# Optimization experiments

Measured on AMD Instinct MI355X. Metric: run time of the kernel, lower is better.

## Reference

```python
import jax, jax.numpy as jnp
import numpy as np

N = 50000        # nodes
E = 800000       # edges
FEAT = 64        # cfg.feature_dim
HID = 128        # cfg.hidden_dim
G = 8            # num graphs
EPS = 1e-5       # LayerNorm eps
MIN_DEPTH, MAX_DEPTH = 0.1, 3.0


def _ln(x, g, b):
    m = jnp.mean(x, axis=-1, keepdims=True)
    v = jnp.mean((x - m) ** 2, axis=-1, keepdims=True)
    return (x - m) * jax.lax.rsqrt(v + EPS) * g + b


def setup_inputs() -> dict:
    key = jax.random.key(0)
    ks = jax.random.split(key, 32)
    f32 = jnp.float32
    inp = {}
    inp['x'] = jax.random.normal(ks[0], (N, FEAT), dtype=f32)
    inp['edge_index'] = jax.random.randint(ks[1], (2, E), 0, N)
    inp['batch'] = jnp.sort(jax.random.randint(ks[2], (N,), 0, G))
    # input_projection: Linear(FEAT,HID) + LayerNorm
    inp['in_w'] = jax.random.normal(ks[3], (FEAT, HID), dtype=f32) * (1.0 / np.sqrt(FEAT))
    inp['in_b'] = jnp.zeros((HID,), f32)
    inp['in_ln_g'] = jnp.ones((HID,), f32)
    inp['in_ln_b'] = jnp.zeros((HID,), f32)
    # epigenetics
    inp['methylation'] = jnp.zeros((HID,), f32)
    inp['histones'] = jnp.zeros((4,), f32)
    inp['log_depth'] = jnp.zeros((), f32)
    # NeuralODEFunc: 3 stacked GCNConv(HID,HID) + LayerNorms, gate MLP, residual scalar
    inp['gcn_w'] = jax.random.normal(ks[4], (3, HID, HID), dtype=f32) * (1.0 / np.sqrt(HID))
    inp['gcn_b'] = jnp.zeros((3, HID), f32)
    inp['ln_g'] = jnp.ones((3, HID), f32)
    inp['ln_b'] = jnp.zeros((3, HID), f32)
    inp['gate_w'] = jax.random.normal(ks[5], (2 * HID, HID), dtype=f32) * (1.0 / np.sqrt(2 * HID))
    inp['gate_b'] = jnp.zeros((HID,), f32)
    inp['residual_weight'] = jnp.asarray(0.1, f32)
    # output_projection: Linear(HID,HID) + LayerNorm
    inp['out_w'] = jax.random.normal(ks[6], (HID, HID), dtype=f32) * (1.0 / np.sqrt(HID))
    inp['out_b'] = jnp.zeros((HID,), f32)
    inp['out_ln_g'] = jnp.ones((HID,), f32)
    inp['out_ln_b'] = jnp.zeros((HID,), f32)
    return inp


def reference(x, edge_index, batch, in_w, in_b, in_ln_g, in_ln_b, methylation,
              histones, log_depth, gcn_w, gcn_b, ln_g, ln_b, gate_w, gate_b,
              residual_weight, out_w, out_b, out_ln_g, out_ln_b):
    n = x.shape[0]
    src, dst = edge_index[0], edge_index[1]

    # input_projection (Dropout is identity in eval)
    h = jax.nn.relu(_ln(x @ in_w + in_b, in_ln_g, in_ln_b))

    # epigenetic regulation (chromatin_accessibility goes through .item() -> constant)
    meth_sil = jnp.mean(jax.nn.sigmoid(methylation))
    hm = jax.nn.sigmoid(histones)
    act = (hm[0] + hm[2]) * 0.5
    rep = (hm[1] + hm[3]) * 0.5
    chrom = jax.lax.stop_gradient(jnp.clip(act - rep + 0.5, 0.0, 1.0))
    h = h * (chrom * (1.0 - meth_sil))

    # symmetric GCN normalization, no self loops (computed once, no grad path)
    deg = jax.ops.segment_sum(jnp.ones((E,), h.dtype), dst, num_segments=n)
    dinv = jnp.where(deg > 0, jax.lax.rsqrt(jnp.maximum(deg, 1.0)), 0.0)
    enorm = (dinv[src] * dinv[dst])[:, None]  # [E,1]

    def gcn(hh, i):
        xw = hh @ gcn_w[i]                                   # [N,H]
        agg = jax.ops.segment_sum(xw[src] * enorm, dst, num_segments=n)
        return agg + gcn_b[i]

    def ode_f(hh):
        h_orig = hh
        cur = hh
        for i in range(3):  # fixed layer count
            h_new = _ln(gcn(cur, i), ln_g[i], ln_b[i])
            if i > 0:
                gate = jax.nn.sigmoid(
                    jnp.concatenate([cur, h_new], axis=-1) @ gate_w + gate_b)
                cur = gate * h_new + (1.0 - gate) * cur
            else:
                cur = h_new
        cur = jnp.tanh(cur)
        return cur + residual_weight * h_orig

    # depth via .item() in torch -> non-differentiable constant
    depth = jax.lax.stop_gradient(
        jnp.clip(jnp.exp(log_depth), MIN_DEPTH, MAX_DEPTH))
    # single fixed RK4 step over t = linspace(0, depth, 2)
    dt = depth
    k1 = ode_f(h)
    k2 = ode_f(h + 0.5 * dt * k1)
    k3 = ode_f(h + 0.5 * dt * k2)
    k4 = ode_f(h + dt * k3)
    h_final = h + (dt / 6.0) * (k1 + 2.0 * k2 + 2.0 * k3 + k4)

    # output_projection + global_mean_pool over batch
    h_out = _ln(h_final @ out_w + out_b, out_ln_g, out_ln_b)
    cnt = jax.ops.segment_sum(jnp.ones((n,), h.dtype), batch, num_segments=G)
    pooled = jax.ops.segment_sum(h_out, batch, num_segments=G)
    return pooled / jnp.maximum(cnt, 1.0)[:, None]
```

## Files before the change

### kernel.cpp

```cpp
#include <hip/hip_runtime.h>
#include <math.h>

#define NN 50000
#define EE 800000
#define HH 128
#define FF 64
#define GG 8
#define PB 500

using short8 = __attribute__((ext_vector_type(8))) short;
using f32x4  = __attribute__((ext_vector_type(4))) float;
using f32x2  = __attribute__((ext_vector_type(2))) float;

__device__ __forceinline__ float sigm(float x){ return 1.0f/(1.0f+expf(-x)); }
__device__ __forceinline__ unsigned short f2bf(float f){
    union { float f; unsigned u; } v; v.f = f;
    unsigned r = v.u + 0x7fff + ((v.u >> 16) & 1);
    return (unsigned short)(r >> 16);
}
__device__ __forceinline__ float bf2f(unsigned short h){
    union { unsigned u; float f; } v; v.u = ((unsigned)h) << 16;
    return v.f;
}

#if __has_builtin(__builtin_amdgcn_cvt_pk_fp8_f32) && __has_builtin(__builtin_amdgcn_cvt_pk_f32_fp8)
#define FP8_HW 1
#else
#define FP8_HW 0
#endif

__device__ __forceinline__ unsigned fp8enc1_sw(float f){
    union { float fl; unsigned u; } x; x.fl = f;
    unsigned s = (x.u >> 31) << 7;
    float a = fabsf(f);
    if (!(a > 0.f)) return s;
    if (a >= 448.f) return s | 0x7E;
    if (a < 0.015625f) {
        int q = (int)(a * 512.f + 0.5f);
        if (q > 7) return s | (1u << 3);
        return s | (unsigned)q;
    }
    unsigned u = x.u + (1u << 19);
    int e32 = (int)((u >> 23) & 255) - 127;
    if (e32 < -6) { int q=(int)(a*512.f+0.5f); if(q>7)q=7; return s|(unsigned)q; }
    if (e32 > 8) return s | 0x7E;
    unsigned m = (u >> 20) & 7;
    return s | ((unsigned)(e32 + 7) << 3) | m;
}
__device__ __forceinline__ float fp8dec1_sw(unsigned v){
    unsigned s = v >> 7, e = (v >> 3) & 15, m = v & 7;
    float f;
    if (e == 0) f = (float)m * 0.001953125f;
    else { union { unsigned u; float fl; } x; x.u = ((e + 120u) << 23) | (m << 20); f = x.fl; }
    return s ? -f : f;
}
__device__ __forceinline__ unsigned char e2fp8(float a){
#if FP8_HW
    return (unsigned char)(__builtin_amdgcn_cvt_pk_fp8_f32(a, a, 0, false) & 0xFF);
#else
    return (unsigned char)fp8enc1_sw(a);
#endif
}
__device__ __forceinline__ unsigned pk4fp8(float a, float b, float c, float d){
#if FP8_HW
    unsigned p0 = (unsigned)__builtin_amdgcn_cvt_pk_fp8_f32(a, b, 0, false);
    unsigned p1 = (unsigned)__builtin_amdgcn_cvt_pk_fp8_f32(c, d, 0, false);
    return (p0 & 0xFFFFu) | ((p1 & 0xFFFFu) << 16);
#else
    return fp8enc1_sw(a) | (fp8enc1_sw(b) << 8) | (fp8enc1_sw(c) << 16) | (fp8enc1_sw(d) << 24);
#endif
}
__device__ __forceinline__ float2 d2fp8(unsigned short u){
#if FP8_HW
    f32x2 r = __builtin_amdgcn_cvt_pk_f32_fp8((int)(unsigned)u, false);
    return make_float2(r[0], r[1]);
#else
    return make_float2(fp8dec1_sw(u & 0xFF), fp8dec1_sw((u >> 8) & 0xFF));
#endif
}

__global__ void k_setup(const float* __restrict__ meth,
                        const float* __restrict__ histones,
                        const float* __restrict__ logd,
                        float* __restrict__ scal)
{
    int l = threadIdx.x;
    float s = sigm(meth[l]) + sigm(meth[l + 64]);
#pragma unroll
    for (int o = 32; o >= 1; o >>= 1) s += __shfl_xor(s, o, 64);
    if (l == 0) {
        float msil = s * (1.0f / 128.0f);
        float h0 = sigm(histones[0]), h1 = sigm(histones[1]);
        float h2 = sigm(histones[2]), h3 = sigm(histones[3]);
        float act = (h0 + h2) * 0.5f, rep = (h1 + h3) * 0.5f;
        float chrom = fminf(fmaxf(act - rep + 0.5f, 0.0f), 1.0f);
        scal[0] = chrom * (1.0f - msil);
        float d = expf(logd[0]);
        scal[1] = fminf(fmaxf(d, 0.1f), 3.0f);
    }
}

__global__ void k_pack(const float* __restrict__ W, unsigned short* __restrict__ out, int K)
{
    int i = blockIdx.x * 256 + threadIdx.x;
    if (i >= K * 128) return;
    int k = i >> 7, n = i & 127;
    int c = k >> 5, kl = k & 31, q = kl >> 3, j = kl & 7;
    int b = n >> 4, ln = n & 15;
    int lane = q * 16 + ln;
    out[((c * 8 + b) * 64 + lane) * 8 + j] = f2bf(W[i]);
}

__global__ void k_cvtx(const float* __restrict__ x, unsigned short* __restrict__ xb)
{
    size_t i = (size_t)blockIdx.x * 256 + threadIdx.x;
    if (i >= (size_t)NN * 16) return;
    float4 v = ((const float4*)x)[i];
    ushort4 o;
    o.x = f2bf(v.x); o.y = f2bf(v.y); o.z = f2bf(v.z); o.w = f2bf(v.w);
    ((ushort4*)xb)[i] = o;
}

__global__ void k_hist(const int* __restrict__ ei, int* __restrict__ hist)
{
    int e = blockIdx.x * 256 + threadIdx.x;
    if (e < EE) atomicAdd(&hist[ei[EE + e]], 1);
}

__global__ void k_dinv(const int* __restrict__ hist, float* __restrict__ dinv)
{
    int n = blockIdx.x * 256 + threadIdx.x;
    if (n < NN) {
        int d = hist[n];
        dinv[n] = d > 0 ? rsqrtf((float)d) : 0.0f;
    }
}

__global__ void k_scan_a(const int* __restrict__ hist, int* __restrict__ aux)
{
    __shared__ int sh[256];
    int b = blockIdx.x, t = threadIdx.x;
    int base = b * 1024 + t * 4;
    int s = 0;
#pragma unroll
    for (int j = 0; j < 4; ++j) { int i = base + j; if (i < NN) s += hist[i]; }
    sh[t] = s; __syncthreads();
    for (int o = 128; o >= 1; o >>= 1) { if (t < o) sh[t] += sh[t + o]; __syncthreads(); }
    if (t == 0) aux[b] = sh[0];
}

__global__ void k_scan_b(int* __restrict__ aux, int nb)
{
    if (blockIdx.x == 0 && threadIdx.x == 0) {
        int run = 0;
        for (int i = 0; i < nb; ++i) { int v = aux[i]; aux[i] = run; run += v; }
    }
}

__global__ void k_scan_c(const int* __restrict__ hist, const int* __restrict__ aux,
                         int* __restrict__ row_ptr)
{
    __shared__ int sh[256];
    int b = blockIdx.x, t = threadIdx.x;
    int base = b * 1024 + t * 4;
    int v[4]; int s = 0;
#pragma unroll
    for (int j = 0; j < 4; ++j) { int i = base + j; v[j] = (i < NN) ? hist[i] : 0; s += v[j]; }
    sh[t] = s; __syncthreads();
    for (int o = 1; o < 256; o <<= 1) {
        int x = 0; if (t >= o) x = sh[t - o];
        __syncthreads(); sh[t] += x; __syncthreads();
    }
    int run = aux[b] + sh[t] - s;
#pragma unroll
    for (int j = 0; j < 4; ++j) { int i = base + j; if (i < NN) row_ptr[i] = run; run += v[j]; }
    if (b == 0 && t == 0) row_ptr[NN] = EE;
}

__global__ void k_scatter(const int* __restrict__ ei, const float* __restrict__ dinv,
                          int* __restrict__ cursor, uint2* __restrict__ ew)
{
    int e = blockIdx.x * 256 + threadIdx.x;
    if (e >= EE) return;
    int s = ei[e], d = ei[EE + e];
    int p = atomicAdd(&cursor[d], 1);
    ew[p] = make_uint2((unsigned)(s & 0xFFFF) | ((unsigned)(d & 15) << 16),
                       __float_as_uint(dinv[s] * dinv[d]));
}

__global__ void k_bounds(const int* __restrict__ batch, int* __restrict__ st)
{
    int g = threadIdx.x;
    if (g > GG) return;
    int lo = 0, hi = NN;
    while (lo < hi) { int mid = (lo + hi) >> 1; if (batch[mid] < g) lo = mid + 1; else hi = mid; }
    st[g] = lo;
}

template<int KC, int MODE>
__global__ __launch_bounds__(256) void k_dense_mfma(
    const unsigned short* __restrict__ A, const unsigned short* __restrict__ Wp,
    const float* __restrict__ bias, const float* __restrict__ lng,
    const float* __restrict__ lnb, const float* __restrict__ scal,
    unsigned short* __restrict__ out, unsigned char* __restrict__ out8)
{
    __shared__ unsigned short Ws[KC * 4096];
    const int t = threadIdx.x;
    {
        const float4* src = (const float4*)Wp;
        float4* dst = (float4*)Ws;
#pragma unroll
        for (int i = 0; i < KC * 2; ++i) dst[t + i * 256] = src[t + i * 256];
    }
    __syncthreads();
    const int wave = t >> 6, lane = t & 63;
    const int quad = lane >> 4, ln = lane & 15;
    const int r0 = blockIdx.x * 64 + wave * 16;
    const int K = KC * 32;
    const int arow = r0 + ln;
    const bool av = arow < NN;

    f32x4 acc[8] = {};
#pragma unroll
    for (int c = 0; c < KC; ++c) {
        short8 a = {};
        if (av) a = *(const short8*)(A + (size_t)arow * K + c * 32 + quad * 8);
#pragma unroll
        for (int b = 0; b < 8; ++b) {
            short8 bb = *(const short8*)&Ws[((c * 8 + b) * 64 + lane) * 8];
            acc[b] = __builtin_amdgcn_mfma_f32_16x16x32_bf16(a, bb, acc[b], 0, 0, 0);
        }
    }

    float b_s[8], g_s[8], e_s[8];
#pragma unroll
    for (int b = 0; b < 8; ++b) {
        int col = b * 16 + ln;
        b_s[b] = bias[col]; g_s[b] = lng[col]; e_s[b] = lnb[col];
    }
    float sc = (MODE == 1) ? scal[0] : 0.0f;
#pragma unroll
    for (int i = 0; i < 4; ++i) {
        int row = r0 + quad * 4 + i;
        float v[8]; float s = 0.f, q = 0.f;
#pragma unroll
        for (int b = 0; b < 8; ++b) { float x = acc[b][i] + b_s[b]; v[b] = x; s += x; q += x * x; }
#pragma unroll
        for (int o = 1; o < 16; o <<= 1) { s += __shfl_xor(s, o, 64); q += __shfl_xor(q, o, 64); }
        float m  = s * (1.0f / 128.0f);
        float vr = q * (1.0f / 128.0f) - m * m;
        float rs = rsqrtf(vr + 1e-5f);
        if (row < NN) {
#pragma unroll
            for (int b = 0; b < 8; ++b) {
                float o2 = (v[b] - m) * rs * g_s[b] + e_s[b];
                if (MODE == 1) o2 = fmaxf(o2, 0.f) * sc;
                out[(size_t)row * 128 + b * 16 + ln] = f2bf(o2);
                if (out8) out8[(size_t)row * 128 + b * 16 + ln] = e2fp8(o2);
            }
        }
    }
}

__global__ __launch_bounds__(128) void k_spgemm(
    const int* __restrict__ rp, const uint2* __restrict__ ew,
    const unsigned char* __restrict__ X8, const unsigned short* __restrict__ Wp,
    const float* __restrict__ bias, const float* __restrict__ lng,
    const float* __restrict__ lnb, unsigned short* __restrict__ out,
    unsigned char* __restrict__ out8)
{
    __shared__ float accf[16 * 132];
    const int t = threadIdx.x, wave = t >> 6, lane = t & 63;
    const int quad = lane >> 4, ln = lane & 15;
    const int n0 = blockIdx.x * 16;
    const int nf = n0 + wave * 8;

    {
        float* z = accf + wave * 8 * 132;
        for (int i = lane; i < 8 * 132; i += 64) z[i] = 0.f;
    }

    if (nf < NN) {
        const int nl = min(nf + 8, NN);
        const int ebeg = __builtin_amdgcn_readfirstlane(rp[nf]);
        const int eend = __builtin_amdgcn_readfirstlane(rp[nl]);
        if (ebeg < eend) {
            float2 r0a = make_float2(0.f, 0.f), r1a = make_float2(0.f, 0.f);
            int curd = (int)((ew[ebeg].x >> 16) & 15u);
            const unsigned char* Xl = X8 + lane * 2;
            uint2 recA[8], recB[8]; float2 gA[8];
#pragma unroll
            for (int u = 0; u < 8; ++u) recA[u] = ew[ebeg + u];
#pragma unroll
            for (int u = 0; u < 8; ++u) recB[u] = ew[ebeg + 8 + u];
#pragma unroll
            for (int u = 0; u < 8; ++u) {
                int src = (int)(recA[u].x & 0xFFFFu);
                gA[u] = d2fp8(*(const unsigned short*)(Xl + (size_t)src * 128));
            }
            for (int e = ebeg; e < eend; e += 8) {
                float2 gB[8];
#pragma unroll
                for (int u = 0; u < 8; ++u) {
                    int src = (int)(recB[u].x & 0xFFFFu);
                    gB[u] = d2fp8(*(const unsigned short*)(Xl + (size_t)src * 128));
                }
                uint2 recC[8];
#pragma unroll
                for (int u = 0; u < 8; ++u) recC[u] = ew[e + 16 + u];
                const int m = min(8, eend - e);
#pragma unroll
                for (int u = 0; u < 8; ++u) {
                    if (u >= m) break;
                    int dl = (int)((recA[u].x >> 16) & 15u);
                    float wt = __uint_as_float(recA[u].y);
                    if (dl != curd) {
                        *(float2*)&accf[curd * 132 + lane * 2] =
                            make_float2(r0a.x + r1a.x, r0a.y + r1a.y);
                        r0a = make_float2(0.f, 0.f);
                        r1a = make_float2(0.f, 0.f);
                        curd = dl;
                    }
                    if (u & 1) {
                        r1a.x = fmaf(wt, gA[u].x, r1a.x);
                        r1a.y = fmaf(wt, gA[u].y, r1a.y);
                    } else {
                        r0a.x = fmaf(wt, gA[u].x, r0a.x);
                        r0a.y = fmaf(wt, gA[u].y, r0a.y);
                    }
                }
#pragma unroll
                for (int u = 0; u < 8; ++u) { recA[u] = recB[u]; recB[u] = recC[u]; gA[u] = gB[u]; }
            }
            *(float2*)&accf[curd * 132 + lane * 2] =
                make_float2(r0a.x + r1a.x, r0a.y + r1a.y);
        }
    }
    __syncthreads();

    f32x4 acc[8] = {};
    const float* ar = accf + (size_t)ln * 132;
#pragma unroll
    for (int c = 0; c < 4; ++c) {
        float4 a0 = *(const float4*)(ar + c * 32 + quad * 8);
        float4 a1 = *(const float4*)(ar + c * 32 + quad * 8 + 4);
        short8 af;
        af[0] = (short)f2bf(a0.x); af[1] = (short)f2bf(a0.y);
        af[2] = (short)f2bf(a0.z); af[3] = (short)f2bf(a0.w);
        af[4] = (short)f2bf(a1.x); af[5] = (short)f2bf(a1.y);
        af[6] = (short)f2bf(a1.z); af[7] = (short)f2bf(a1.w);
#pragma unroll
        for (int b = 0; b < 8; ++b) {
            short8 bb = *(const short8*)(Wp + ((size_t)(c * 8 + b) * 64 + lane) * 8);
            acc[b] = __builtin_amdgcn_mfma_f32_16x16x32_bf16(af, bb, acc[b], 0, 0, 0);
        }
    }

    float b_s[8], g_s[8], e_s[8];
#pragma unroll
    for (int b = 0; b < 8; ++b) {
        int col = b * 16 + ln;
        b_s[b] = bias[col]; g_s[b] = lng[col]; e_s[b] = lnb[col];
    }
#pragma unroll
    for (int i = 0; i < 4; ++i) {
        int row = n0 + quad * 4 + i;
        float v[8]; float s = 0.f, q = 0.f;
#pragma unroll
        for (int b = 0; b < 8; ++b) { float x = acc[b][i] + b_s[b]; v[b] = x; s += x; q += x * x; }
#pragma unroll
        for (int o = 1; o < 16; o <<= 1) { s += __shfl_xor(s, o, 64); q += __shfl_xor(q, o, 64); }
        float m  = s * (1.0f / 128.0f);
        float vr = q * (1.0f / 128.0f) - m * m;
        float rs = rsqrtf(vr + 1e-5f);
        if (((quad >> 1) == wave) && row < NN) {
#pragma unroll
            for (int b = 0; b < 8; ++b) {
                float o2 = (v[b] - m) * rs * g_s[b] + e_s[b];
                out[(size_t)row * 128 + b * 16 + ln] = f2bf(o2);
                if (out8) out8[(size_t)row * 128 + b * 16 + ln] = e2fp8(o2);
            }
        }
    }
}

__global__ __launch_bounds__(256) void k_gate_mfma(
    unsigned short* __restrict__ cur, const unsigned short* __restrict__ hnew,
    const unsigned short* __restrict__ Wp, const float* __restrict__ gb,
    unsigned char* __restrict__ cur8)
{
    __shared__ unsigned short Ws[16384];
    const int t = threadIdx.x;
    const int wave = t >> 6, lane = t & 63;
    const int quad = lane >> 4, ln = lane & 15;
    const int r0 = blockIdx.x * 64 + wave * 16;
    const int arow = r0 + ln;
    const bool av = arow < NN;

    f32x4 acc[8] = {};
#pragma unroll
    for (int s = 0; s < 2; ++s) {
        __syncthreads();
        {
            const float4* src = (const float4*)(Wp + (size_t)s * 16384);
            float4* dst = (float4*)Ws;
#pragma unroll
            for (int i = 0; i < 8; ++i) dst[t + i * 256] = src[t + i * 256];
        }
        __syncthreads();
        const unsigned short* A = s ? hnew : cur;
#pragma unroll
        for (int c = 0; c < 4; ++c) {
            short8 a = {};
            if (av) a = *(const short8*)(A + (size_t)arow * 128 + c * 32 + quad * 8);
#pragma unroll
            for (int b = 0; b < 8; ++b) {
                short8 bb = *(const short8*)&Ws[((c * 8 + b) * 64 + lane) * 8];
                acc[b] = __builtin_amdgcn_mfma_f32_16x16x32_bf16(a, bb, acc[b], 0, 0, 0);
            }
        }
    }

    float gb_s[8];
#pragma unroll
    for (int b = 0; b < 8; ++b) gb_s[b] = gb[b * 16 + ln];
#pragma unroll
    for (int i = 0; i < 4; ++i) {
        int row = r0 + quad * 4 + i;
        if (row < NN) {
#pragma unroll
            for (int b = 0; b < 8; ++b) {
                size_t idx = (size_t)row * 128 + b * 16 + ln;
                float g  = sigm(acc[b][i] + gb_s[b]);
                float cu = bf2f(cur[idx]);
                float hn = bf2f(hnew[idx]);
                float r  = g * hn + (1.f - g) * cu;
                cur[idx]  = f2bf(r);
                cur8[idx] = e2fp8(r);
            }
        }
    }
}

template<int S>
__global__ __launch_bounds__(256) void k_stage(
    const unsigned short* __restrict__ cur, const unsigned short* __restrict__ fin,
    const unsigned short* __restrict__ h0, float* __restrict__ acc,
    unsigned short* __restrict__ ybuf, const float* __restrict__ scal,
    const float* __restrict__ rwp, unsigned char* __restrict__ y8)
{
    size_t i = (size_t)blockIdx.x * 256 + threadIdx.x;
    if (i >= (size_t)NN * 32) return;
    float dt = scal[1], rw = rwp[0];
    float wk = (S == 1 || S == 4) ? dt * (1.f / 6.f) : dt * (1.f / 3.f);
    ushort4 c4 = ((const ushort4*)cur)[i];
    ushort4 f4 = ((const ushort4*)fin)[i];
    ushort4 h4 = ((const ushort4*)h0)[i];
    float tv[4];
    tv[0] = tanhf(bf2f(c4.x)) + rw * bf2f(f4.x);
    tv[1] = tanhf(bf2f(c4.y)) + rw * bf2f(f4.y);
    tv[2] = tanhf(bf2f(c4.z)) + rw * bf2f(f4.z);
    tv[3] = tanhf(bf2f(c4.w)) + rw * bf2f(f4.w);
    float4 a;
    if (S == 1) { a.x = wk*tv[0]; a.y = wk*tv[1]; a.z = wk*tv[2]; a.w = wk*tv[3]; }
    else {
        a = ((const float4*)acc)[i];
        a.x += wk*tv[0]; a.y += wk*tv[1]; a.z += wk*tv[2]; a.w += wk*tv[3];
    }
    ((float4*)acc)[i] = a;
    float h[4] = { bf2f(h4.x), bf2f(h4.y), bf2f(h4.z), bf2f(h4.w) };
    float yv[4];
    if (S == 4) {
        yv[0] = h[0] + a.x; yv[1] = h[1] + a.y; yv[2] = h[2] + a.z; yv[3] = h[3] + a.w;
    } else {
        float cn = (S == 3) ? dt : 0.5f * dt;
        yv[0] = h[0] + cn*tv[0]; yv[1] = h[1] + cn*tv[1];
        yv[2] = h[2] + cn*tv[2]; yv[3] = h[3] + cn*tv[3];
    }
    ushort4 y;
    y.x = f2bf(yv[0]); y.y = f2bf(yv[1]); y.z = f2bf(yv[2]); y.w = f2bf(yv[3]);
    ((ushort4*)ybuf)[i] = y;
    ((unsigned*)y8)[i] = pk4fp8(yv[0], yv[1], yv[2], yv[3]);
}

__global__ __launch_bounds__(128) void k_pool1(
    const unsigned short* __restrict__ h, const int* __restrict__ batch,
    float* __restrict__ partial)
{
    int c = threadIdx.x, b = blockIdx.x;
    int r0 = b * (NN / PB), r1 = r0 + (NN / PB);
    float acc = 0.f; int g = batch[r0];
#pragma unroll 4
    for (int r = r0; r < r1; ++r) {
        int gg = batch[r];
        if (gg != g) { partial[(size_t)b * 1024 + g * 128 + c] = acc; acc = 0.f; g = gg; }
        acc += bf2f(h[(size_t)r * 128 + c]);
    }
    partial[(size_t)b * 1024 + g * 128 + c] = acc;
}

__global__ __launch_bounds__(256) void k_pool2(
    const float* __restrict__ partial, const int* __restrict__ st,
    float* __restrict__ out)
{
    __shared__ float sh[8][32];
    int cb = blockIdx.x & 3, g = blockIdx.x >> 2;
    int cl = threadIdx.x & 31, sl = threadIdx.x >> 5;
    int c = cb * 32 + cl;
    float s = 0.f;
    for (int b = sl; b < PB; b += 8) s += partial[(size_t)b * 1024 + g * 128 + c];
    sh[sl][cl] = s; __syncthreads();
    if (sl == 0) {
        float tt = 0.f;
#pragma unroll
        for (int i = 0; i < 8; ++i) tt += sh[i][cl];
        int cnt = st[g + 1] - st[g];
        out[g * 128 + c] = tt / (float)(cnt > 0 ? cnt : 1);
    }
}

static inline size_t al(size_t x) { return (x + 255) & ~(size_t)255; }

extern "C" void kernel_launch(void* const* d_in, const int* in_sizes, int n_in,
                              void* d_out, int out_size, void* d_ws, size_t ws_size,
                              hipStream_t stream)
{
    const float* x       = (const float*)d_in[0];
    const int*   ei      = (const int*)d_in[1];
    const int*   batch   = (const int*)d_in[2];
    const float* in_w    = (const float*)d_in[3];
    const float* in_b    = (const float*)d_in[4];
    const float* in_lng  = (const float*)d_in[5];
    const float* in_lnb  = (const float*)d_in[6];
    const float* meth    = (const float*)d_in[7];
    const float* histn   = (const float*)d_in[8];
    const float* logd    = (const float*)d_in[9];
    const float* gcn_w   = (const float*)d_in[10];
    const float* gcn_b   = (const float*)d_in[11];
    const float* ln_g    = (const float*)d_in[12];
    const float* ln_b    = (const float*)d_in[13];
    const float* gate_w  = (const float*)d_in[14];
    const float* gate_b  = (const float*)d_in[15];
    const float* rw      = (const float*)d_in[16];
    const float* out_w   = (const float*)d_in[17];
    const float* out_b   = (const float*)d_in[18];
    const float* out_lng = (const float*)d_in[19];
    const float* out_lnb = (const float*)d_in[20];
    float* out = (float*)d_out;

    char* w = (char*)d_ws;
    size_t off = 0;
    float* scal   = (float*)(w + off); off += al(16 * 4);
    int*   hist   = (int*)(w + off);   off += al((size_t)NN * 4);
    int*   rp     = (int*)(w + off);   off += al((size_t)(NN + 1) * 4);
    int*   cursor = (int*)(w + off);   off += al((size_t)(NN + 1) * 4);
    int*   aux    = (int*)(w + off);   off += al(64 * 4);
    int*   st     = (int*)(w + off);   off += al(16 * 4);
    float* dinv   = (float*)(w + off); off += al((size_t)NN * 4);
    uint2* ew     = (uint2*)(w + off); off += al((size_t)(EE + 32) * 8);
    float* partial= (float*)(w + off); off += al((size_t)PB * 1024 * 4);
    unsigned short* inwp  = (unsigned short*)(w + off); off += al(64 * 128 * 2);
    unsigned short* gcnwp = (unsigned short*)(w + off); off += al((size_t)3 * 128 * 128 * 2);
    unsigned short* gwp   = (unsigned short*)(w + off); off += al((size_t)2 * 128 * 128 * 2);
    unsigned short* owp   = (unsigned short*)(w + off); off += al(128 * 128 * 2);
    size_t B16 = al((size_t)NN * 128 * 2);
    unsigned short* xb  = (unsigned short*)(w + off); off += al((size_t)NN * 64 * 2);
    unsigned short* h0  = (unsigned short*)(w + off); off += B16;
    unsigned short* y   = (unsigned short*)(w + off); off += B16;
    unsigned short* cur = (unsigned short*)(w + off); off += B16;
    unsigned short* t2  = (unsigned short*)(w + off); off += B16;
    float* acc = (float*)(w + off); off += al((size_t)NN * 128 * 4);
    size_t B8 = al((size_t)NN * 128);
    unsigned char* h08  = (unsigned char*)(w + off); off += B8;
    unsigned char* y8   = (unsigned char*)(w + off); off += B8;
    unsigned char* cur8 = (unsigned char*)(w + off); off += B8;
    if (off > ws_size) return;

    hipMemsetAsync(hist, 0, (size_t)NN * 4, stream);
    hipMemsetAsync(partial, 0, (size_t)PB * 1024 * 4, stream);
    hipMemsetAsync(ew + EE, 0, 32 * sizeof(uint2), stream);

    k_setup<<<1, 64, 0, stream>>>(meth, histn, logd, scal);
    k_pack<<<32, 256, 0, stream>>>(in_w, inwp, 64);
    for (int i = 0; i < 3; ++i)
        k_pack<<<64, 256, 0, stream>>>(gcn_w + (size_t)i * 128 * 128,
                                       gcnwp + (size_t)i * 128 * 128, 128);
    k_pack<<<64, 256, 0, stream>>>(gate_w, gwp, 128);
    k_pack<<<64, 256, 0, stream>>>(gate_w + 128 * 128, gwp + 128 * 128, 128);
    k_pack<<<64, 256, 0, stream>>>(out_w, owp, 128);
    k_cvtx<<<3125, 256, 0, stream>>>(x, xb);

    k_hist<<<(EE + 255) / 256, 256, 0, stream>>>(ei, hist);
    k_dinv<<<(NN + 255) / 256, 256, 0, stream>>>(hist, dinv);
    k_scan_a<<<49, 256, 0, stream>>>(hist, aux);
    k_scan_b<<<1, 1, 0, stream>>>(aux, 49);
    k_scan_c<<<49, 256, 0, stream>>>(hist, aux, rp);
    hipMemcpyAsync(cursor, rp, (size_t)(NN + 1) * 4, hipMemcpyDeviceToDevice, stream);
    k_scatter<<<(EE + 255) / 256, 256, 0, stream>>>(ei, dinv, cursor, ew);
    k_bounds<<<1, 16, 0, stream>>>(batch, st);

    const int DG = (NN + 63) / 64;
    const int SG = (NN + 15) / 16;
    k_dense_mfma<2, 1><<<DG, 256, 0, stream>>>(xb, inwp, in_b, in_lng, in_lnb, scal, h0, h08);

    for (int s = 1; s <= 4; ++s) {
        const unsigned short* fin = (s == 1) ? h0 : y;
        const unsigned char*  fin8 = (s == 1) ? h08 : y8;
        k_spgemm<<<SG, 128, 0, stream>>>(rp, ew, fin8, gcnwp, gcn_b, ln_g, ln_b, cur, cur8);
        for (int i = 1; i <= 2; ++i) {
            k_spgemm<<<SG, 128, 0, stream>>>(rp, ew, cur8,
                                             gcnwp + (size_t)i * 128 * 128, gcn_b + i * 128,
                                             ln_g + i * 128, ln_b + i * 128, t2, (unsigned char*)0);
            k_gate_mfma<<<DG, 256, 0, stream>>>(cur, t2, gwp, gate_b, cur8);
        }
        if (s == 1)      k_stage<1><<<6250, 256, 0, stream>>>(cur, fin, h0, acc, y, scal, rw, y8);
        else if (s == 2) k_stage<2><<<6250, 256, 0, stream>>>(cur, fin, h0, acc, y, scal, rw, y8);
        else if (s == 3) k_stage<3><<<6250, 256, 0, stream>>>(cur, fin, h0, acc, y, scal, rw, y8);
        else             k_stage<4><<<6250, 256, 0, stream>>>(cur, fin, h0, acc, y, scal, rw, y8);
    }

    k_dense_mfma<4, 0><<<DG, 256, 0, stream>>>(y, owp, out_b, out_lng, out_lnb, scal, t2, (unsigned char*)0);
    k_pool1<<<PB, 128, 0, stream>>>(t2, batch, partial);
    k_pool2<<<GG * 4, 256, 0, stream>>>(partial, st, out);
}
```

Baseline: 923.9 us.

## Merge setup launches and partition edge scatter by destination range

Folds the seven weight-pack launches into one kernel writing a contiguous packed buffer, and moves the graph-bounds search into a second block of the setup kernel. It also replaces two memsets by having the pool and scatter kernels write their zeros themselves. The scatter kernel now has each block scan a chunk of edges but handle only destinations in one of eight node ranges, so atomics and writes stay localised. The cost is that each edge index gets read eight times. Overall the aim is fewer launches and better locality in the CSR build.

```diff
diff --git a/kernel.cpp b/kernel.cpp
--- a/kernel.cpp
+++ b/kernel.cpp
@@ -7,6 +7,7 @@
 #define FF 64
 #define GG 8
 #define PB 500
+#define SB 1600
 
 using short8 = __attribute__((ext_vector_type(8))) short;
 using f32x4  = __attribute__((ext_vector_type(4))) float;
@@ -82,8 +83,17 @@
 __global__ void k_setup(const float* __restrict__ meth,
                         const float* __restrict__ histones,
                         const float* __restrict__ logd,
-                        float* __restrict__ scal)
-{
+                        float* __restrict__ scal,
+                        const int* __restrict__ batch, int* __restrict__ st)
+{
+    if (blockIdx.x == 1) {
+        int g = threadIdx.x;
+        if (g > GG) return;
+        int lo = 0, hi = NN;
+        while (lo < hi) { int mid = (lo + hi) >> 1; if (batch[mid] < g) lo = mid + 1; else hi = mid; }
+        st[g] = lo;
+        return;
+    }
     int l = threadIdx.x;
     float s = sigm(meth[l]) + sigm(meth[l + 64]);
 #pragma unroll
@@ -100,15 +110,27 @@
     }
 }
 
-__global__ void k_pack(const float* __restrict__ W, unsigned short* __restrict__ out, int K)
+__global__ void k_packall(const float* __restrict__ in_w, const float* __restrict__ gcn_w,
+                          const float* __restrict__ gate_w, const float* __restrict__ out_w,
+                          unsigned short* __restrict__ outp)
 {
     int i = blockIdx.x * 256 + threadIdx.x;
-    if (i >= K * 128) return;
-    int k = i >> 7, n = i & 127;
-    int c = k >> 5, kl = k & 31, q = kl >> 3, j = kl & 7;
+    if (i >= 8192 + 6 * 16384) return;
+    const float* src; int base, li;
+    if (i < 8192) { src = in_w + i; base = 0; li = i; }
+    else {
+        int j = i - 8192;
+        int m = j >> 14, r = j & 16383;
+        base = 8192 + (m << 14); li = r;
+        if (m < 3)      src = gcn_w  + m * 16384 + r;
+        else if (m < 5) src = gate_w + (m - 3) * 16384 + r;
+        else            src = out_w + r;
+    }
+    int k = li >> 7, n = li & 127;
+    int c = k >> 5, kl = k & 31, q = kl >> 3, j2 = kl & 7;
     int b = n >> 4, ln = n & 15;
     int lane = q * 16 + ln;
-    out[((c * 8 + b) * 64 + lane) * 8 + j] = f2bf(W[i]);
+    outp[base + ((c * 8 + b) * 64 + lane) * 8 + j2] = f2bf(*src);
 }
 
 __global__ void k_cvtx(const float* __restrict__ x, unsigned short* __restrict__ xb)
@@ -177,24 +199,26 @@
     if (b == 0 && t == 0) row_ptr[NN] = EE;
 }
 
-__global__ void k_scatter(const int* __restrict__ ei, const float* __restrict__ dinv,
+__global__ __launch_bounds__(256) void k_scatter(const int* __restrict__ ei,
+                          const float* __restrict__ dinv,
                           int* __restrict__ cursor, uint2* __restrict__ ew)
 {
-    int e = blockIdx.x * 256 + threadIdx.x;
-    if (e >= EE) return;
-    int s = ei[e], d = ei[EE + e];
-    int p = atomicAdd(&cursor[d], 1);
-    ew[p] = make_uint2((unsigned)(s & 0xFFFF) | ((unsigned)(d & 15) << 16),
-                       __float_as_uint(dinv[s] * dinv[d]));
-}
-
-__global__ void k_bounds(const int* __restrict__ batch, int* __restrict__ st)
-{
-    int g = threadIdx.x;
-    if (g > GG) return;
-    int lo = 0, hi = NN;
-    while (lo < hi) { int mid = (lo + hi) >> 1; if (batch[mid] < g) lo = mid + 1; else hi = mid; }
-    st[g] = lo;
+    if (blockIdx.x == 0 && threadIdx.x < 32)
+        ew[EE + threadIdx.x] = make_uint2(0u, 0u);
+    const int grp = blockIdx.x & 7;
+    const int blk = blockIdx.x >> 3;
+    const int CH  = EE / (SB / 8);
+    const int e0 = blk * CH, e1 = e0 + CH;
+    const int glo = grp * (NN / 8), ghi = glo + (NN / 8);
+    for (int e = e0 + threadIdx.x; e < e1; e += 256) {
+        int d = ei[EE + e];
+        if (d >= glo && d < ghi) {
+            int s = ei[e];
+            int p = atomicAdd(&cursor[d], 1);
+            ew[p] = make_uint2((unsigned)(s & 0xFFFF) | ((unsigned)(d & 15) << 16),
+                               __float_as_uint(dinv[s] * dinv[d]));
+        }
+    }
 }
 
 template<int KC, int MODE>
@@ -489,14 +513,21 @@
 {
     int c = threadIdx.x, b = blockIdx.x;
     int r0 = b * (NN / PB), r1 = r0 + (NN / PB);
-    float acc = 0.f; int g = batch[r0];
+    float acc = 0.f;
+    int gfirst = batch[r0], g = gfirst;
 #pragma unroll 4
     for (int r = r0; r < r1; ++r) {
         int gg = batch[r];
-        if (gg != g) { partial[(size_t)b * 1024 + g * 128 + c] = acc; acc = 0.f; g = gg; }
+        if (gg != g) {
+            partial[(size_t)b * 1024 + g * 128 + c] = acc;
+            for (int z = g + 1; z < gg; ++z) partial[(size_t)b * 1024 + z * 128 + c] = 0.f;
+            acc = 0.f; g = gg;
+        }
         acc += bf2f(h[(size_t)r * 128 + c]);
     }
     partial[(size_t)b * 1024 + g * 128 + c] = acc;
+    for (int z = 0; z < gfirst; ++z)  partial[(size_t)b * 1024 + z * 128 + c] = 0.f;
+    for (int z = g + 1; z < GG; ++z)  partial[(size_t)b * 1024 + z * 128 + c] = 0.f;
 }
 
 __global__ __launch_bounds__(256) void k_pool2(
@@ -559,10 +590,11 @@
     float* dinv   = (float*)(w + off); off += al((size_t)NN * 4);
     uint2* ew     = (uint2*)(w + off); off += al((size_t)(EE + 32) * 8);
     float* partial= (float*)(w + off); off += al((size_t)PB * 1024 * 4);
-    unsigned short* inwp  = (unsigned short*)(w + off); off += al(64 * 128 * 2);
-    unsigned short* gcnwp = (unsigned short*)(w + off); off += al((size_t)3 * 128 * 128 * 2);
-    unsigned short* gwp   = (unsigned short*)(w + off); off += al((size_t)2 * 128 * 128 * 2);
-    unsigned short* owp   = (unsigned short*)(w + off); off += al(128 * 128 * 2);
+    unsigned short* wpak = (unsigned short*)(w + off); off += al((size_t)(8192 + 6 * 16384) * 2);
+    unsigned short* inwp  = wpak;
+    unsigned short* gcnwp = wpak + 8192;
+    unsigned short* gwp   = wpak + 8192 + 3 * 16384;
+    unsigned short* owp   = wpak + 8192 + 5 * 16384;
     size_t B16 = al((size_t)NN * 128 * 2);
     unsigned short* xb  = (unsigned short*)(w + off); off += al((size_t)NN * 64 * 2);
     unsigned short* h0  = (unsigned short*)(w + off); off += B16;
@@ -577,17 +609,9 @@
     if (off > ws_size) return;
 
     hipMemsetAsync(hist, 0, (size_t)NN * 4, stream);
-    hipMemsetAsync(partial, 0, (size_t)PB * 1024 * 4, stream);
-    hipMemsetAsync(ew + EE, 0, 32 * sizeof(uint2), stream);
-
-    k_setup<<<1, 64, 0, stream>>>(meth, histn, logd, scal);
-    k_pack<<<32, 256, 0, stream>>>(in_w, inwp, 64);
-    for (int i = 0; i < 3; ++i)
-        k_pack<<<64, 256, 0, stream>>>(gcn_w + (size_t)i * 128 * 128,
-                                       gcnwp + (size_t)i * 128 * 128, 128);
-    k_pack<<<64, 256, 0, stream>>>(gate_w, gwp, 128);
-    k_pack<<<64, 256, 0, stream>>>(gate_w + 128 * 128, gwp + 128 * 128, 128);
-    k_pack<<<64, 256, 0, stream>>>(out_w, owp, 128);
+
+    k_setup<<<2, 64, 0, stream>>>(meth, histn, logd, scal, batch, st);
+    k_packall<<<(8192 + 6 * 16384 + 255) / 256, 256, 0, stream>>>(in_w, gcn_w, gate_w, out_w, wpak);
     k_cvtx<<<3125, 256, 0, stream>>>(x, xb);
 
     k_hist<<<(EE + 255) / 256, 256, 0, stream>>>(ei, hist);
@@ -596,8 +620,7 @@
     k_scan_b<<<1, 1, 0, stream>>>(aux, 49);
     k_scan_c<<<49, 256, 0, stream>>>(hist, aux, rp);
     hipMemcpyAsync(cursor, rp, (size_t)(NN + 1) * 4, hipMemcpyDeviceToDevice, stream);
-    k_scatter<<<(EE + 255) / 256, 256, 0, stream>>>(ei, dinv, cursor, ew);
-    k_bounds<<<1, 16, 0, stream>>>(batch, st);
+    k_scatter<<<SB, 256, 0, stream>>>(ei, dinv, cursor, ew);
 
     const int DG = (NN + 63) / 64;
     const int SG = (NN + 15) / 16;
```

New measurement: 901.9 us. -2.4%, faster.
